# Kernel tuning notes

Measured on AMD Instinct MI355X. Metric: run time of the kernel, lower is better.

The kernel has to match this reference:

```python
import jax, jax.numpy as jnp
import numpy as np

HEADS = 8
DIM_HEAD = 64
SCALE = DIM_HEAD ** -0.5


def setup_inputs() -> dict:
    key = jax.random.key(0)
    ks = jax.random.split(key, 6)
    B, S, D = 4, 2048, 512
    return {
        "hidden_states": jax.random.normal(ks[0], (B, S, D), jnp.float32),
        "Wq": jax.random.normal(ks[1], (D, D), jnp.float32) * (D ** -0.5),
        "Wk": jax.random.normal(ks[2], (D, D), jnp.float32) * (D ** -0.5),
        "Wv": jax.random.normal(ks[3], (D, D), jnp.float32) * (D ** -0.5),
        "Wo": jax.random.normal(ks[4], (D, D), jnp.float32) * (D ** -0.5),
        "bo": jnp.zeros((D,), jnp.float32),
    }


def reference(hidden_states, Wq, Wk, Wv, Wo, bo):
    B, S, D = hidden_states.shape
    H, Dh = HEADS, DIM_HEAD
    # Linear projections (torch Linear: x @ W.T; weights here stored as [D, D] used directly)
    q = hidden_states @ Wq  # [B,S,D]
    k = hidden_states @ Wk
    v = hidden_states @ Wv
    # head_to_batch_dim: [B,S,D] -> [B,H,S,Dh]
    q = q.reshape(B, S, H, Dh).transpose(0, 2, 1, 3)
    k = k.reshape(B, S, H, Dh).transpose(0, 2, 1, 3)
    v = v.reshape(B, S, H, Dh).transpose(0, 2, 1, 3)
    # scaled dot-product attention, scores materialized as in baddbmm path
    scores = jnp.einsum("bhqd,bhkd->bhqk", q, k) * SCALE  # [B,H,S,S]
    probs = jax.nn.softmax(scores, axis=-1)
    out = jnp.einsum("bhqk,bhkd->bhqd", probs, v)  # [B,H,S,Dh]
    # batch_to_head_dim: [B,H,S,Dh] -> [B,S,D]
    out = out.transpose(0, 2, 1, 3).reshape(B, S, D)
    # output projection (Dropout with p=0 is identity)
    return out @ Wo + bo
```

## Files before the change

kernel.cpp:

```cpp
#include <hip/hip_runtime.h>
#include <cstdint>
#include <cstddef>


typedef __bf16 bf16;
typedef __bf16 bf16x4_t __attribute__((ext_vector_type(4)));
typedef __bf16 bf16x8_t __attribute__((ext_vector_type(8)));
typedef float  floatx4  __attribute__((ext_vector_type(4)));
typedef short  shortx4  __attribute__((ext_vector_type(4)));
typedef uint32_t u32x4  __attribute__((ext_vector_type(4)));

#define NB   4
#define SEQ  2048
#define DM   512
#define NH   8
#define DH   64
#define MTOT (NB * SEQ)


__device__ __forceinline__ void gload16(const void* g, void* l) {
    __builtin_amdgcn_global_load_lds((const __attribute__((address_space(1))) unsigned int*)g,
                                     (__attribute__((address_space(3))) unsigned int*)l,
                                     16, 0, 0);
}

__device__ __forceinline__ shortx4 pack4(floatx4 v) {
    union { bf16x4_t h; shortx4 s; } u;
    u.h = (bf16x4_t){ (bf16)v[0], (bf16)v[1], (bf16)v[2], (bf16)v[3] };
    return u.s;
}

__global__ __launch_bounds__(256) void prep(
        const float* __restrict__ X, const float* __restrict__ Wq, const float* __restrict__ Wk,
        const float* __restrict__ Wv, const float* __restrict__ Wo,
        bf16* __restrict__ xb, bf16* __restrict__ Wqkvt, bf16* __restrict__ Wot) {
    __shared__ float T[64][65];
    const int tid = threadIdx.x;
    const int bx = blockIdx.x;
    if (bx < 4096) {
        int i = (bx * 256 + tid) * 4;
        float4 v = *(const float4*)(X + i);
        bf16x4_t o = { (bf16)v.x, (bf16)v.y, (bf16)v.z, (bf16)v.w };
        *(bf16x4_t*)(xb + i) = o;
        return;
    }
    const int idx = bx - 4096;
    const int m = idx >> 6;
    const int k0 = ((idx >> 3) & 7) * 64, n0 = (idx & 7) * 64;
    const float* W = (m == 0) ? Wq : (m == 1) ? Wk : (m == 2) ? Wv : Wo;
    const float scale = (m == 0) ? 0.18033688011112042f : 1.0f;
#pragma unroll
    for (int p = 0; p < 4; p++) {
        int row = p * 16 + (tid >> 4), col = (tid & 15) * 4;
        float4 v = *(const float4*)(W + (size_t)(k0 + row) * DM + n0 + col);
        T[row][col + 0] = v.x * scale; T[row][col + 1] = v.y * scale;
        T[row][col + 2] = v.z * scale; T[row][col + 3] = v.w * scale;
    }
    __syncthreads();
#pragma unroll
    for (int p = 0; p < 4; p++) {
        int nr = p * 16 + (tid >> 4), kc = (tid & 15) * 4;
        bf16x4_t o = { (bf16)T[kc][nr], (bf16)T[kc + 1][nr], (bf16)T[kc + 2][nr], (bf16)T[kc + 3][nr] };
        bf16* dst = (m < 3) ? (Wqkvt + ((size_t)(m * DM + n0 + nr)) * DM + k0 + kc)
                            : (Wot + (size_t)(n0 + nr) * DM + k0 + kc);
        *(bf16x4_t*)dst = o;
    }
}

__global__ __launch_bounds__(256) void gemm_qkv(
        const bf16* __restrict__ A, const bf16* __restrict__ Bt,
        bf16* __restrict__ Qh, bf16* __restrict__ Kh, bf16* __restrict__ Vt) {
    __shared__ __attribute__((aligned(16))) bf16 Sm[2][128 * 64];
    bf16* As = Sm[0]; bf16* Bs = Sm[1];
    const int tid = threadIdx.x;
    const int wave = tid >> 6, lane = tid & 63;
    const int l15 = lane & 15, quad = lane >> 4, h7 = l15 & 7;
    const int m0 = blockIdx.x * 128, n0 = blockIdx.y * 128;
    const int mw = (wave >> 1) * 64, nw = (wave & 1) * 64;
    const int srow = lane >> 3, sc = (lane & 7) ^ srow;

    floatx4 zero = {0.f, 0.f, 0.f, 0.f};
    floatx4 acc[4][4];
#pragma unroll
    for (int i = 0; i < 4; i++)
#pragma unroll
        for (int j = 0; j < 4; j++) acc[i][j] = zero;

    for (int k0 = 0; k0 < DM; k0 += 64) {
#pragma unroll
        for (int t = 0; t < 4; t++) {
            int row = wave * 32 + t * 8 + srow;
            gload16(A  + (size_t)(m0 + row) * DM + k0 + sc * 8, As + (wave * 32 + t * 8) * 64);
            gload16(Bt + (size_t)(n0 + row) * DM + k0 + sc * 8, Bs + (wave * 32 + t * 8) * 64);
        }
        __syncthreads();
#pragma unroll
        for (int ks = 0; ks < 2; ks++) {
            bf16x8_t af[4], bfr[4];
#pragma unroll
            for (int i = 0; i < 4; i++)
                af[i] = *(const bf16x8_t*)(As + (mw + i * 16 + l15) * 64 + (((ks * 4 + quad) ^ h7) * 8));
#pragma unroll
            for (int j = 0; j < 4; j++)
                bfr[j] = *(const bf16x8_t*)(Bs + (nw + j * 16 + l15) * 64 + (((ks * 4 + quad) ^ h7) * 8));
#pragma unroll
            for (int i = 0; i < 4; i++)
#pragma unroll
                for (int j = 0; j < 4; j++)
                    acc[i][j] = __builtin_amdgcn_mfma_f32_16x16x32_bf16(af[i], bfr[j], acc[i][j], 0, 0, 0);
        }
        __syncthreads();
    }

    bf16* E = (bf16*)Sm;
    const int sect = n0 >> 9;
    const int bq = m0 >> 11;
    if (sect != 2) {
        bf16* dstbase = (sect == 0) ? Qh : Kh;
#pragma unroll
        for (int p = 0; p < 2; p++) {
            if ((wave >> 1) == p) {
#pragma unroll
                for (int i = 0; i < 4; i++)
#pragma unroll
                    for (int j = 0; j < 4; j++)
#pragma unroll
                        for (int r = 0; r < 4; r++)
                            E[(i * 16 + quad * 4 + r) * 136 + nw + j * 16 + l15] = (bf16)acc[i][j][r];
            }
            __syncthreads();
#pragma unroll
            for (int pp = 0; pp < 4; pp++) {
                int idx = pp * 256 + tid;
                int rowl = idx >> 4, chunk = idx & 15;
                u32x4 v = *(const u32x4*)(E + rowl * 136 + chunk * 8);
                int mm = m0 + p * 64 + rowl;
                int s = mm & (SEQ - 1);
                int n = n0 + chunk * 8;
                int h = (n >> 6) & 7, d = n & 63;
                *(u32x4*)(dstbase + (((size_t)(bq * NH + h)) * SEQ + s) * DH + d) = v;
            }
            __syncthreads();
        }
    } else {
#pragma unroll
        for (int p = 0; p < 2; p++) {
            if ((wave & 1) == p) {
#pragma unroll
                for (int i = 0; i < 4; i++)
#pragma unroll
                    for (int j = 0; j < 4; j++)
                        *(shortx4*)(E + (j * 16 + l15) * 136 + mw + i * 16 + quad * 4) = pack4(acc[i][j]);
            }
            __syncthreads();
#pragma unroll
            for (int pp = 0; pp < 4; pp++) {
                int idx = pp * 256 + tid;
                int rowl = idx >> 4, chunk = idx & 15;
                u32x4 v = *(const u32x4*)(E + rowl * 136 + chunk * 8);
                int n = n0 + p * 64 + rowl;
                int h = (n >> 6) & 7, d = n & 63;
                int s = (m0 & (SEQ - 1)) + chunk * 8;
                *(u32x4*)(Vt + (((size_t)(bq * NH + h)) * DH + d) * SEQ + s) = v;
            }
            __syncthreads();
        }
    }
}

__global__ __launch_bounds__(256) void gemm_out(
        const bf16* __restrict__ A, const bf16* __restrict__ Bt,
        const float* __restrict__ bo, float* __restrict__ out) {
    __shared__ __attribute__((aligned(16))) bf16 As[64 * 64];
    __shared__ __attribute__((aligned(16))) bf16 Bs[128 * 64];
    const int tid = threadIdx.x;
    const int wave = tid >> 6, lane = tid & 63;
    const int l15 = lane & 15, quad = lane >> 4, h7 = l15 & 7;
    const int m0 = blockIdx.x * 64, n0 = blockIdx.y * 128;
    const int nw = wave * 32;
    const int srow = lane >> 3, sc = (lane & 7) ^ srow;

    floatx4 zero = {0.f, 0.f, 0.f, 0.f};
    floatx4 acc[4][2];
#pragma unroll
    for (int i = 0; i < 4; i++)
#pragma unroll
        for (int j = 0; j < 2; j++) acc[i][j] = zero;

    for (int k0 = 0; k0 < DM; k0 += 64) {
#pragma unroll
        for (int t = 0; t < 2; t++) {
            int row = wave * 16 + t * 8 + srow;
            gload16(A + (size_t)(m0 + row) * DM + k0 + sc * 8, As + (wave * 16 + t * 8) * 64);
        }
#pragma unroll
        for (int t = 0; t < 4; t++) {
            int row = wave * 32 + t * 8 + srow;
            gload16(Bt + (size_t)(n0 + row) * DM + k0 + sc * 8, Bs + (wave * 32 + t * 8) * 64);
        }
        __syncthreads();
#pragma unroll
        for (int ks = 0; ks < 2; ks++) {
            bf16x8_t af[4], bfr[2];
#pragma unroll
            for (int i = 0; i < 4; i++)
                af[i] = *(const bf16x8_t*)(As + (i * 16 + l15) * 64 + (((ks * 4 + quad) ^ h7) * 8));
#pragma unroll
            for (int j = 0; j < 2; j++)
                bfr[j] = *(const bf16x8_t*)(Bs + (nw + j * 16 + l15) * 64 + (((ks * 4 + quad) ^ h7) * 8));
#pragma unroll
            for (int i = 0; i < 4; i++)
#pragma unroll
                for (int j = 0; j < 2; j++)
                    acc[i][j] = __builtin_amdgcn_mfma_f32_16x16x32_bf16(af[i], bfr[j], acc[i][j], 0, 0, 0);
        }
        __syncthreads();
    }
#pragma unroll
    for (int i = 0; i < 4; i++)
#pragma unroll
        for (int j = 0; j < 2; j++)
#pragma unroll
            for (int r = 0; r < 4; r++) {
                int m = m0 + i * 16 + quad * 4 + r;
                int n = n0 + nw + j * 16 + l15;
                out[(size_t)m * DM + n] = acc[i][j][r] + bo[n];
            }
}

__global__ __launch_bounds__(256, 2) void flash_attn(
        const bf16* __restrict__ Q, const bf16* __restrict__ Kh,
        const bf16* __restrict__ Vt, bf16* __restrict__ Ob) {
    __shared__ __attribute__((aligned(16))) bf16 SMEM[4 * 8192];
    const int tid = threadIdx.x;
    const int wave = tid >> 6, lane = tid & 63;
    const int l15 = lane & 15, quad = lane >> 4, h7 = l15 & 7;
    const int qh = wave >> 1, kvh = wave & 1;
    const int qt = blockIdx.x & 15, bh = blockIdx.x >> 4;
    const int q0 = qt * 128;
    const bf16* Kb = Kh + (size_t)bh * SEQ * DH;
    const bf16* Vb = Vt + (size_t)bh * DH * SEQ;

    bf16x8_t aq[4][2];
#pragma unroll
    for (int sub = 0; sub < 4; sub++) {
        const bf16* qr = Q + ((size_t)bh * SEQ + q0 + qh * 64 + sub * 16 + l15) * DH;
        aq[sub][0] = *(const bf16x8_t*)(qr + quad * 8);
        aq[sub][1] = *(const bf16x8_t*)(qr + 32 + quad * 8);
    }

    const int srow = lane >> 3, sc = (lane & 7) ^ srow;
    auto stage = [&](int buf, int kv0) {
#pragma unroll
        for (int t = 0; t < 2; t++) {
            int rb = wave * 16 + t * 8;
            gload16(Kb + (size_t)(kv0 + rb + srow) * DH + sc * 8, SMEM + buf * 8192 + rb * 64);
            gload16(Vb + (size_t)(rb + srow) * SEQ + kv0 + sc * 8, SMEM + buf * 8192 + 4096 + rb * 64);
        }
    };

    floatx4 zero = {0.f, 0.f, 0.f, 0.f};
    floatx4 oacc[4][4];
    float l_run[4] = {0.f, 0.f, 0.f, 0.f};
#pragma unroll
    for (int sub = 0; sub < 4; sub++)
#pragma unroll
        for (int d = 0; d < 4; d++) oacc[sub][d] = zero;

    stage(0, 0);
    stage(1, 64);
    for (int seg = 0; seg < 16; seg++) {
        __syncthreads();
        if (seg < 15) {
            stage((2 * seg + 2) & 3, (2 * seg + 2) * 64);
            stage((2 * seg + 3) & 3, (2 * seg + 3) * 64);
        }
#pragma unroll
        for (int half = 0; half < 2; half++) {
            const bf16* Ks = SMEM + ((2 * seg + half) & 3) * 8192;
            const bf16* Vs = Ks + 4096;
            floatx4 st[4][2];
#pragma unroll
            for (int nsl = 0; nsl < 2; nsl++) {
                int row = (kvh * 2 + nsl) * 16 + l15;
                const bf16* kr = Ks + row * 64;
                bf16x8_t k0 = *(const bf16x8_t*)(kr + ((quad ^ h7) * 8));
                bf16x8_t k1 = *(const bf16x8_t*)(kr + (((4 + quad) ^ h7) * 8));
#pragma unroll
                for (int sub = 0; sub < 4; sub++) {
                    floatx4 a = zero;
                    a = __builtin_amdgcn_mfma_f32_16x16x32_bf16(k0, aq[sub][0], a, 0, 0, 0);
                    a = __builtin_amdgcn_mfma_f32_16x16x32_bf16(k1, aq[sub][1], a, 0, 0, 0);
                    st[sub][nsl] = a;
                }
            }
#pragma unroll
            for (int sub = 0; sub < 4; sub++) {
                float s = 0.f;
#pragma unroll
                for (int nsl = 0; nsl < 2; nsl++)
#pragma unroll
                    for (int r = 0; r < 4; r++) {
                        float p = __builtin_amdgcn_exp2f(st[sub][nsl][r]);
                        st[sub][nsl][r] = p;
                        s += p;
                    }
                l_run[sub] += s;
            }
#pragma unroll
            for (int cl = 0; cl < 2; cl++) {
                int c = kvh * 2 + cl;
                shortx4 ap[4];
#pragma unroll
                for (int sub = 0; sub < 4; sub++) ap[sub] = pack4(st[sub][cl]);
                int cc = 2 * c + (quad >> 1);
#pragma unroll
                for (int d = 0; d < 4; d++) {
                    const bf16* vr = Vs + (d * 16 + l15) * 64;
                    shortx4 bv = *(const shortx4*)(vr + ((cc ^ h7) * 8) + (quad & 1) * 4);
#pragma unroll
                    for (int sub = 0; sub < 4; sub++)
                        oacc[sub][d] = __builtin_amdgcn_mfma_f32_16x16x16bf16_1k(ap[sub], bv, oacc[sub][d], 0, 0, 0);
                }
            }
        }
    }

    float lf[4];
#pragma unroll
    for (int sub = 0; sub < 4; sub++) {
        float l = l_run[sub];
        l += __shfl_xor(l, 16, 64);
        l += __shfl_xor(l, 32, 64);
        lf[sub] = l;
    }
    __syncthreads();
    float* blob = (float*)SMEM + qh * (68 * 64);
    if (kvh == 1) {
#pragma unroll
        for (int sub = 0; sub < 4; sub++)
#pragma unroll
            for (int d = 0; d < 4; d++)
#pragma unroll
                for (int r = 0; r < 4; r++)
                    blob[((sub * 4 + d) * 4 + r) * 64 + lane] = oacc[sub][d][r];
#pragma unroll
        for (int sub = 0; sub < 4; sub++)
            blob[(64 + sub) * 64 + lane] = lf[sub];
    }
    __syncthreads();
    if (kvh == 0) {
#pragma unroll
        for (int sub = 0; sub < 4; sub++)
#pragma unroll
            for (int d = 0; d < 4; d++)
#pragma unroll
                for (int r = 0; r < 4; r++)
                    oacc[sub][d][r] += blob[((sub * 4 + d) * 4 + r) * 64 + lane];
#pragma unroll
        for (int sub = 0; sub < 4; sub++)
            lf[sub] += blob[(64 + sub) * 64 + lane];

        const int b = bh >> 3, h = bh & 7;
#pragma unroll
        for (int sub = 0; sub < 4; sub++) {
            float linv[4];
#pragma unroll
            for (int r = 0; r < 4; r++) linv[r] = 1.0f / __shfl(lf[sub], quad * 4 + r, 64);
#pragma unroll
            for (int d = 0; d < 4; d++)
#pragma unroll
                for (int r = 0; r < 4; r++) {
                    int s = q0 + qh * 64 + sub * 16 + quad * 4 + r;
                    Ob[((size_t)b * SEQ + s) * DM + h * DH + d * 16 + l15] = (bf16)(oacc[sub][d][r] * linv[r]);
                }
        }
    }
}

extern "C" void kernel_launch(void* const* d_in, const int* in_sizes, int n_in,
                              void* d_out, int out_size, void* d_ws, size_t ws_size,
                              hipStream_t stream) {
    const float* X  = (const float*)d_in[0];
    const float* Wq = (const float*)d_in[1];
    const float* Wk = (const float*)d_in[2];
    const float* Wv = (const float*)d_in[3];
    const float* Wo = (const float*)d_in[4];
    const float* bo = (const float*)d_in[5];
    float* out = (float*)d_out;

    char* ws = (char*)d_ws;
    bf16* Xb    = (bf16*)(ws + 0);
    bf16* Wqkvt = (bf16*)(ws + 8388608);
    bf16* Wot   = (bf16*)(ws + 9961472);
    bf16* Qh    = (bf16*)(ws + 10485760);
    bf16* Kh    = (bf16*)(ws + 18874368);
    bf16* Vt    = (bf16*)(ws + 27262976);
    bf16* Ob    = (bf16*)(ws + 35651584);

    prep<<<4096 + 256, 256, 0, stream>>>(X, Wq, Wk, Wv, Wo, Xb, Wqkvt, Wot);
    gemm_qkv<<<dim3(MTOT / 128, 1536 / 128), 256, 0, stream>>>(Xb, Wqkvt, Qh, Kh, Vt);
    flash_attn<<<NB * NH * (SEQ / 128), 256, 0, stream>>>(Qh, Kh, Vt, Ob);
    gemm_out<<<dim3(MTOT / 64, DM / 128), 256, 0, stream>>>(Ob, Wot, bo, out);
}
```

Measured before the change: 159.3 us.

## Double-buffer LDS tiles in QKV and output GEMMs, single-pass QKV epilogue

Both projection GEMMs now use two LDS stages. The next K-tile's global-to-LDS loads are issued right after the barrier, so they overlap with the MFMA work on the current tile, and the trailing per-iteration barrier is dropped. The larger LDS allocation also lets the QKV epilogue stage the whole 128x128 output tile in one pass instead of two half passes, which removes two barriers. The cost is more LDS per block (64KB in gemm_qkv), which may cut occupancy. The attention kernel, probably the main cost, is unchanged.

```diff
diff --git a/kernel.cpp b/kernel.cpp
--- a/kernel.cpp
+++ b/kernel.cpp
@@ -70,8 +70,7 @@
 __global__ __launch_bounds__(256) void gemm_qkv(
         const bf16* __restrict__ A, const bf16* __restrict__ Bt,
         bf16* __restrict__ Qh, bf16* __restrict__ Kh, bf16* __restrict__ Vt) {
-    __shared__ __attribute__((aligned(16))) bf16 Sm[2][128 * 64];
-    bf16* As = Sm[0]; bf16* Bs = Sm[1];
+    __shared__ __attribute__((aligned(16))) bf16 AB[2][2][128 * 64];
     const int tid = threadIdx.x;
     const int wave = tid >> 6, lane = tid & 63;
     const int l15 = lane & 15, quad = lane >> 4, h7 = l15 & 7;
@@ -79,6 +78,15 @@
     const int mw = (wave >> 1) * 64, nw = (wave & 1) * 64;
     const int srow = lane >> 3, sc = (lane & 7) ^ srow;
 
+    auto stage = [&](int buf, int k0) {
+#pragma unroll
+        for (int t = 0; t < 4; t++) {
+            int rb = wave * 32 + t * 8;
+            gload16(A  + (size_t)(m0 + rb + srow) * DM + k0 + sc * 8, AB[buf][0] + rb * 64);
+            gload16(Bt + (size_t)(n0 + rb + srow) * DM + k0 + sc * 8, AB[buf][1] + rb * 64);
+        }
+    };
+
     floatx4 zero = {0.f, 0.f, 0.f, 0.f};
     floatx4 acc[4][4];
 #pragma unroll
@@ -86,14 +94,12 @@
 #pragma unroll
         for (int j = 0; j < 4; j++) acc[i][j] = zero;
 
-    for (int k0 = 0; k0 < DM; k0 += 64) {
-#pragma unroll
-        for (int t = 0; t < 4; t++) {
-            int row = wave * 32 + t * 8 + srow;
-            gload16(A  + (size_t)(m0 + row) * DM + k0 + sc * 8, As + (wave * 32 + t * 8) * 64);
-            gload16(Bt + (size_t)(n0 + row) * DM + k0 + sc * 8, Bs + (wave * 32 + t * 8) * 64);
-        }
+    stage(0, 0);
+    for (int kt = 0; kt < DM / 64; kt++) {
         __syncthreads();
+        if (kt + 1 < DM / 64) stage((kt + 1) & 1, (kt + 1) * 64);
+        const bf16* As = AB[kt & 1][0];
+        const bf16* Bs = AB[kt & 1][1];
 #pragma unroll
         for (int ks = 0; ks < 2; ks++) {
             bf16x8_t af[4], bfr[4];
@@ -109,61 +115,48 @@
                 for (int j = 0; j < 4; j++)
                     acc[i][j] = __builtin_amdgcn_mfma_f32_16x16x32_bf16(af[i], bfr[j], acc[i][j], 0, 0, 0);
         }
-        __syncthreads();
-    }
-
-    bf16* E = (bf16*)Sm;
+    }
+
+    bf16* E = (bf16*)AB;
     const int sect = n0 >> 9;
     const int bq = m0 >> 11;
+    __syncthreads();
     if (sect != 2) {
         bf16* dstbase = (sect == 0) ? Qh : Kh;
 #pragma unroll
-        for (int p = 0; p < 2; p++) {
-            if ((wave >> 1) == p) {
-#pragma unroll
-                for (int i = 0; i < 4; i++)
-#pragma unroll
-                    for (int j = 0; j < 4; j++)
-#pragma unroll
-                        for (int r = 0; r < 4; r++)
-                            E[(i * 16 + quad * 4 + r) * 136 + nw + j * 16 + l15] = (bf16)acc[i][j][r];
-            }
-            __syncthreads();
-#pragma unroll
-            for (int pp = 0; pp < 4; pp++) {
-                int idx = pp * 256 + tid;
-                int rowl = idx >> 4, chunk = idx & 15;
-                u32x4 v = *(const u32x4*)(E + rowl * 136 + chunk * 8);
-                int mm = m0 + p * 64 + rowl;
-                int s = mm & (SEQ - 1);
-                int n = n0 + chunk * 8;
-                int h = (n >> 6) & 7, d = n & 63;
-                *(u32x4*)(dstbase + (((size_t)(bq * NH + h)) * SEQ + s) * DH + d) = v;
-            }
-            __syncthreads();
+        for (int i = 0; i < 4; i++)
+#pragma unroll
+            for (int j = 0; j < 4; j++)
+#pragma unroll
+                for (int r = 0; r < 4; r++)
+                    E[(mw + i * 16 + quad * 4 + r) * 136 + nw + j * 16 + l15] = (bf16)acc[i][j][r];
+        __syncthreads();
+#pragma unroll
+        for (int pp = 0; pp < 8; pp++) {
+            int idx = pp * 256 + tid;
+            int rowl = idx >> 4, chunk = idx & 15;
+            u32x4 v = *(const u32x4*)(E + rowl * 136 + chunk * 8);
+            int s = (m0 + rowl) & (SEQ - 1);
+            int n = n0 + chunk * 8;
+            int h = (n >> 6) & 7, d = n & 63;
+            *(u32x4*)(dstbase + (((size_t)(bq * NH + h)) * SEQ + s) * DH + d) = v;
         }
     } else {
 #pragma unroll
-        for (int p = 0; p < 2; p++) {
-            if ((wave & 1) == p) {
-#pragma unroll
-                for (int i = 0; i < 4; i++)
-#pragma unroll
-                    for (int j = 0; j < 4; j++)
-                        *(shortx4*)(E + (j * 16 + l15) * 136 + mw + i * 16 + quad * 4) = pack4(acc[i][j]);
-            }
-            __syncthreads();
-#pragma unroll
-            for (int pp = 0; pp < 4; pp++) {
-                int idx = pp * 256 + tid;
-                int rowl = idx >> 4, chunk = idx & 15;
-                u32x4 v = *(const u32x4*)(E + rowl * 136 + chunk * 8);
-                int n = n0 + p * 64 + rowl;
-                int h = (n >> 6) & 7, d = n & 63;
-                int s = (m0 & (SEQ - 1)) + chunk * 8;
-                *(u32x4*)(Vt + (((size_t)(bq * NH + h)) * DH + d) * SEQ + s) = v;
-            }
-            __syncthreads();
+        for (int i = 0; i < 4; i++)
+#pragma unroll
+            for (int j = 0; j < 4; j++)
+                *(shortx4*)(E + (nw + j * 16 + l15) * 136 + mw + i * 16 + quad * 4) = pack4(acc[i][j]);
+        __syncthreads();
+#pragma unroll
+        for (int pp = 0; pp < 8; pp++) {
+            int idx = pp * 256 + tid;
+            int rowl = idx >> 4, chunk = idx & 15;
+            u32x4 v = *(const u32x4*)(E + rowl * 136 + chunk * 8);
+            int n = n0 + rowl;
+            int h = (n >> 6) & 7, d = n & 63;
+            int s = (m0 & (SEQ - 1)) + chunk * 8;
+            *(u32x4*)(Vt + (((size_t)(bq * NH + h)) * DH + d) * SEQ + s) = v;
         }
     }
 }
@@ -171,8 +164,8 @@
 __global__ __launch_bounds__(256) void gemm_out(
         const bf16* __restrict__ A, const bf16* __restrict__ Bt,
         const float* __restrict__ bo, float* __restrict__ out) {
-    __shared__ __attribute__((aligned(16))) bf16 As[64 * 64];
-    __shared__ __attribute__((aligned(16))) bf16 Bs[128 * 64];
+    __shared__ __attribute__((aligned(16))) bf16 Ao[2][64 * 64];
+    __shared__ __attribute__((aligned(16))) bf16 Bo[2][128 * 64];
     const int tid = threadIdx.x;
     const int wave = tid >> 6, lane = tid & 63;
     const int l15 = lane & 15, quad = lane >> 4, h7 = l15 & 7;
@@ -180,6 +173,19 @@
     const int nw = wave * 32;
     const int srow = lane >> 3, sc = (lane & 7) ^ srow;
 
+    auto stage = [&](int buf, int k0) {
+#pragma unroll
+        for (int t = 0; t < 2; t++) {
+            int rb = wave * 16 + t * 8;
+            gload16(A + (size_t)(m0 + rb + srow) * DM + k0 + sc * 8, Ao[buf] + rb * 64);
+        }
+#pragma unroll
+        for (int t = 0; t < 4; t++) {
+            int rb = wave * 32 + t * 8;
+            gload16(Bt + (size_t)(n0 + rb + srow) * DM + k0 + sc * 8, Bo[buf] + rb * 64);
+        }
+    };
+
     floatx4 zero = {0.f, 0.f, 0.f, 0.f};
     floatx4 acc[4][2];
 #pragma unroll
@@ -187,18 +193,12 @@
 #pragma unroll
         for (int j = 0; j < 2; j++) acc[i][j] = zero;
 
-    for (int k0 = 0; k0 < DM; k0 += 64) {
-#pragma unroll
-        for (int t = 0; t < 2; t++) {
-            int row = wave * 16 + t * 8 + srow;
-            gload16(A + (size_t)(m0 + row) * DM + k0 + sc * 8, As + (wave * 16 + t * 8) * 64);
-        }
-#pragma unroll
-        for (int t = 0; t < 4; t++) {
-            int row = wave * 32 + t * 8 + srow;
-            gload16(Bt + (size_t)(n0 + row) * DM + k0 + sc * 8, Bs + (wave * 32 + t * 8) * 64);
-        }
+    stage(0, 0);
+    for (int kt = 0; kt < DM / 64; kt++) {
         __syncthreads();
+        if (kt + 1 < DM / 64) stage((kt + 1) & 1, (kt + 1) * 64);
+        const bf16* As = Ao[kt & 1];
+        const bf16* Bs = Bo[kt & 1];
 #pragma unroll
         for (int ks = 0; ks < 2; ks++) {
             bf16x8_t af[4], bfr[2];
@@ -214,7 +214,6 @@
                 for (int j = 0; j < 2; j++)
                     acc[i][j] = __builtin_amdgcn_mfma_f32_16x16x32_bf16(af[i], bfr[j], acc[i][j], 0, 0, 0);
         }
-        __syncthreads();
     }
 #pragma unroll
     for (int i = 0; i < 4; i++)
```

Result: faster. 148.8 us (-6.6%).
